# Kernel optimization log

Hardware: AMD Instinct MI355X
Metric: run time of the kernel (lower is better)

The kernel has to match this reference:

```python
import jax, jax.numpy as jnp
import numpy as np

N_NODES = 100000
N_EDGES = 1600000
IN_DIM = 128
HID = 128
OUT = 40


def setup_inputs() -> dict:
    key = jax.random.key(0)
    ks = jax.random.split(key, 8)
    x = jax.random.normal(ks[0], (N_NODES, IN_DIM), dtype=jnp.float32)
    edge_index = jax.random.randint(ks[1], (2, N_EDGES), 0, N_NODES, dtype=jnp.int64)
    def glorot(k, fan_in, fan_out):
        s = jnp.sqrt(6.0 / (fan_in + fan_out)).astype(jnp.float32)
        return jax.random.uniform(k, (fan_in, fan_out), jnp.float32, -s, s)
    return {
        "x": x,
        "edge_index": edge_index,
        "W1": glorot(ks[2], IN_DIM, HID), "b1": jnp.zeros((HID,), jnp.float32),
        "W2": glorot(ks[3], HID, HID),    "b2": jnp.zeros((HID,), jnp.float32),
        "W3": glorot(ks[4], HID, HID),    "b3": jnp.zeros((HID,), jnp.float32),
        "Wl": glorot(ks[5], HID, OUT),    "bl": jnp.zeros((OUT,), jnp.float32),
    }


def _gcn_norm(edge_index, num_nodes):
    # PyG GCNConv default: add self-loops, symmetric normalization.
    loops = jnp.arange(num_nodes, dtype=edge_index.dtype)
    src = jnp.concatenate([edge_index[0], loops])
    dst = jnp.concatenate([edge_index[1], loops])
    deg = jax.ops.segment_sum(jnp.ones_like(dst, dtype=jnp.float32), dst,
                              num_segments=num_nodes)
    dis = jnp.where(deg > 0, jax.lax.rsqrt(deg), 0.0)  # deg^{-1/2}
    norm = dis[src] * dis[dst]  # [E+N]
    return src, dst, norm


def _gcn_conv(x, W, b, src, dst, norm, num_nodes):
    h = x @ W                                   # [N, F_out]
    msg = h[src] * norm[:, None]                # gather + scale
    out = jax.ops.segment_sum(msg, dst, num_segments=num_nodes)
    return out + b


def reference(x, edge_index, W1, b1, W2, b2, W3, b3, Wl, bl):
    n = x.shape[0]
    src, dst, norm = _gcn_norm(edge_index, n)
    h = jax.nn.relu(_gcn_conv(x, W1, b1, src, dst, norm, n))
    h = jax.nn.relu(_gcn_conv(h, W2, b2, src, dst, norm, n))
    h = _gcn_conv(h, W3, b3, src, dst, norm, n)
    # dropout p=0.5 is identity in eval mode
    return h @ Wl + bl
```

## Files before the change

### kernel.cpp

```cpp
#include <hip/hip_runtime.h>

typedef __attribute__((ext_vector_type(8))) short sh8;
typedef __attribute__((ext_vector_type(4))) float f4;

__device__ __forceinline__ float bf2f(unsigned short u) {
    union { unsigned int u; float f; } c; c.u = ((unsigned int)u) << 16; return c.f;
}
__device__ __forceinline__ unsigned short f2bf(float f) {
    union { float f; unsigned int u; } c; c.f = f;
    unsigned int x = c.u;
    unsigned int r = (x + 0x7fffu + ((x >> 16) & 1u)) >> 16;
    return (unsigned short)r;
}
__device__ __forceinline__ void bfsplit(float x, short& hi, short& lo) {
    unsigned short h = f2bf(x);
    float r = x - bf2f(h);
    hi = (short)h;
    lo = (short)f2bf(r);
}

__global__ void k_zero_cnt(int* cnt, int N) {
    int i = blockIdx.x * 256 + threadIdx.x;
    if (i < N) cnt[i] = 0;
}

__global__ void k_count(const int* __restrict__ dst, int* __restrict__ cnt,
                        int* __restrict__ rank, int E, int N) {
    int E4 = E >> 2;
    for (int i = blockIdx.x * 256 + threadIdx.x; i < E4; i += gridDim.x * 256) {
        int4 d = ((const int4*)dst)[i];
        int4 r;
        r.x = ((unsigned)d.x < (unsigned)N) ? atomicAdd(&cnt[d.x], 1) : -1;
        r.y = ((unsigned)d.y < (unsigned)N) ? atomicAdd(&cnt[d.y], 1) : -1;
        r.z = ((unsigned)d.z < (unsigned)N) ? atomicAdd(&cnt[d.z], 1) : -1;
        r.w = ((unsigned)d.w < (unsigned)N) ? atomicAdd(&cnt[d.w], 1) : -1;
        ((int4*)rank)[i] = r;
    }
    if (blockIdx.x == 0) {
        for (int e = (E4 << 2) + threadIdx.x; e < E; e += 256) {
            int d = dst[e];
            rank[e] = ((unsigned)d < (unsigned)N) ? atomicAdd(&cnt[d], 1) : -1;
        }
    }
}

#define SCAN_B 256
__global__ void k_scan_a(const int* __restrict__ cnt, int* __restrict__ rowptr,
                         int* __restrict__ bsum, float* __restrict__ dis, int N) {
    __shared__ int sh[SCAN_B];
    int t = threadIdx.x, i = blockIdx.x * SCAN_B + t;
    int v = (i < N) ? cnt[i] : 0;
    if (i < N) dis[i] = rsqrtf((float)(v + 1));
    sh[t] = v; __syncthreads();
    for (int off = 1; off < SCAN_B; off <<= 1) {
        int x = (t >= off) ? sh[t - off] : 0;
        __syncthreads();
        sh[t] += x;
        __syncthreads();
    }
    int incl = sh[t];
    if (i < N) rowptr[i] = incl - v;
    if (t == SCAN_B - 1) bsum[blockIdx.x] = incl;
}

__global__ void k_scan_b(int* bsum, int NB) {
    __shared__ int sh[512];
    int t = threadIdx.x;
    int v = (t < NB) ? bsum[t] : 0;
    sh[t] = v; __syncthreads();
    for (int off = 1; off < 512; off <<= 1) {
        int x = (t >= off) ? sh[t - off] : 0;
        __syncthreads();
        sh[t] += x;
        __syncthreads();
    }
    if (t < NB) bsum[t] = sh[t] - v;
}

__global__ void k_scan_c(int* __restrict__ rowptr, const int* __restrict__ bsum, int N) {
    int i = blockIdx.x * 256 + threadIdx.x;
    if (i < N) rowptr[i] += bsum[blockIdx.x];
}

__global__ void k_fill(const int* __restrict__ src, const int* __restrict__ dst,
                       const int* __restrict__ rank, const int* __restrict__ rowptr,
                       int* __restrict__ csrc, int E, int N) {
    int E4 = E >> 2;
    for (int i = blockIdx.x * 256 + threadIdx.x; i < E4; i += gridDim.x * 256) {
        int4 d4 = ((const int4*)dst)[i];
        int4 s4 = ((const int4*)src)[i];
        int4 r4 = ((const int4*)rank)[i];
        #pragma unroll
        for (int q = 0; q < 4; ++q) {
            int d = (q == 0) ? d4.x : (q == 1) ? d4.y : (q == 2) ? d4.z : d4.w;
            int s = (q == 0) ? s4.x : (q == 1) ? s4.y : (q == 2) ? s4.z : s4.w;
            int r = (q == 0) ? r4.x : (q == 1) ? r4.y : (q == 2) ? r4.z : r4.w;
            if ((unsigned)d >= (unsigned)N || (unsigned)s >= (unsigned)N || r < 0) continue;
            csrc[rowptr[d] + r] = s;
        }
    }
    if (blockIdx.x == 0) {
        for (int e = (E4 << 2) + threadIdx.x; e < E; e += 256) {
            int d = dst[e];
            int s = src[e];
            int r = rank[e];
            if ((unsigned)d >= (unsigned)N || (unsigned)s >= (unsigned)N || r < 0) continue;
            csrc[rowptr[d] + r] = s;
        }
    }
}

__global__ __launch_bounds__(256)
void k_gemm128_a32(const float* __restrict__ X,
                   const float* __restrict__ W,
                   const float* __restrict__ dis,
                   unsigned short* __restrict__ H, int nPairs) {
    int wave = threadIdx.x >> 6;
    int lane = threadIdx.x & 63;
    int ln = lane & 15, quad = lane >> 4;
    int c0 = (wave & 1) * 64;
    int subTile = wave >> 1;

    sh8 bh[4][4], blo[4][4];
    #pragma unroll
    for (int nt = 0; nt < 4; ++nt) {
        int col = c0 + nt * 16 + ln;
        #pragma unroll
        for (int kt = 0; kt < 4; ++kt) {
            int k0 = kt * 32 + quad * 8;
            #pragma unroll
            for (int j = 0; j < 8; ++j) {
                short h, l;
                bfsplit(W[(k0 + j) * 128 + col], h, l);
                bh[nt][kt][j] = h; blo[nt][kt][j] = l;
            }
        }
    }

    for (int p = blockIdx.x; p < nPairs; p += gridDim.x) {
        int nodeBase = p * 32 + subTile * 16;
        const float* xrow = X + (nodeBase + ln) * 128 + quad * 8;
        sh8 ah[4], al[4];
        #pragma unroll
        for (int kt = 0; kt < 4; ++kt) {
            f4 v0 = *(const f4*)(xrow + kt * 32);
            f4 v1 = *(const f4*)(xrow + kt * 32 + 4);
            #pragma unroll
            for (int j = 0; j < 4; ++j) {
                short h, l;
                bfsplit(v0[j], h, l); ah[kt][j] = h; al[kt][j] = l;
                bfsplit(v1[j], h, l); ah[kt][j + 4] = h; al[kt][j + 4] = l;
            }
        }

        f4 acc[4] = { {0.f,0.f,0.f,0.f}, {0.f,0.f,0.f,0.f}, {0.f,0.f,0.f,0.f}, {0.f,0.f,0.f,0.f} };
        #pragma unroll
        for (int kt = 0; kt < 4; ++kt)
            #pragma unroll
            for (int nt = 0; nt < 4; ++nt) {
                acc[nt] = __builtin_amdgcn_mfma_f32_16x16x32_bf16(ah[kt], bh[nt][kt], acc[nt], 0, 0, 0);
                acc[nt] = __builtin_amdgcn_mfma_f32_16x16x32_bf16(ah[kt], blo[nt][kt], acc[nt], 0, 0, 0);
                acc[nt] = __builtin_amdgcn_mfma_f32_16x16x32_bf16(al[kt], bh[nt][kt], acc[nt], 0, 0, 0);
            }

        float ds[4];
        #pragma unroll
        for (int r = 0; r < 4; ++r) ds[r] = dis[nodeBase + quad * 4 + r];
        #pragma unroll
        for (int nt = 0; nt < 4; ++nt) {
            int col = c0 + nt * 16 + ln;
            #pragma unroll
            for (int r = 0; r < 4; ++r)
                H[(nodeBase + quad * 4 + r) * 128 + col] = f2bf(acc[nt][r] * ds[r]);
        }
    }
}

__global__ __launch_bounds__(256)
void k_gemm128_a16(const unsigned short* __restrict__ X,
                   const float* __restrict__ W,
                   const float* __restrict__ dis,
                   unsigned short* __restrict__ H, int nPairs) {
    int wave = threadIdx.x >> 6;
    int lane = threadIdx.x & 63;
    int ln = lane & 15, quad = lane >> 4;
    int c0 = (wave & 1) * 64;
    int subTile = wave >> 1;

    sh8 bh[4][4], blo[4][4];
    #pragma unroll
    for (int nt = 0; nt < 4; ++nt) {
        int col = c0 + nt * 16 + ln;
        #pragma unroll
        for (int kt = 0; kt < 4; ++kt) {
            int k0 = kt * 32 + quad * 8;
            #pragma unroll
            for (int j = 0; j < 8; ++j) {
                short h, l;
                bfsplit(W[(k0 + j) * 128 + col], h, l);
                bh[nt][kt][j] = h; blo[nt][kt][j] = l;
            }
        }
    }

    for (int p = blockIdx.x; p < nPairs; p += gridDim.x) {
        int nodeBase = p * 32 + subTile * 16;
        const unsigned short* xrow = X + (nodeBase + ln) * 128 + quad * 8;
        sh8 a[4];
        #pragma unroll
        for (int kt = 0; kt < 4; ++kt) a[kt] = *(const sh8*)(xrow + kt * 32);

        f4 acc[4] = { {0.f,0.f,0.f,0.f}, {0.f,0.f,0.f,0.f}, {0.f,0.f,0.f,0.f}, {0.f,0.f,0.f,0.f} };
        #pragma unroll
        for (int kt = 0; kt < 4; ++kt)
            #pragma unroll
            for (int nt = 0; nt < 4; ++nt) {
                acc[nt] = __builtin_amdgcn_mfma_f32_16x16x32_bf16(a[kt], bh[nt][kt], acc[nt], 0, 0, 0);
                acc[nt] = __builtin_amdgcn_mfma_f32_16x16x32_bf16(a[kt], blo[nt][kt], acc[nt], 0, 0, 0);
            }

        float ds[4];
        #pragma unroll
        for (int r = 0; r < 4; ++r) ds[r] = dis[nodeBase + quad * 4 + r];
        #pragma unroll
        for (int nt = 0; nt < 4; ++nt) {
            int col = c0 + nt * 16 + ln;
            #pragma unroll
            for (int r = 0; r < 4; ++r)
                H[(nodeBase + quad * 4 + r) * 128 + col] = f2bf(acc[nt][r] * ds[r]);
        }
    }
}

__global__ __launch_bounds__(256)
void k_agg(const unsigned short* __restrict__ H,
           unsigned short* __restrict__ O,
           const float* __restrict__ dis,
           const int* __restrict__ rowptr,
           const int* __restrict__ cnt,
           const int* __restrict__ csrc,
           const float* __restrict__ bias,
           int relu, int N) {
    int n = (blockIdx.x * 256 + threadIdx.x) >> 5;
    if (n >= N) return;
    int lane = threadIdx.x & 31;
    int sub  = lane & 15;
    int half = lane >> 4;

    float a0 = 0.f, a1 = 0.f, a2 = 0.f, a3 = 0.f;
    float a4 = 0.f, a5 = 0.f, a6 = 0.f, a7 = 0.f;

    auto addrow = [&](uint4 v) {
        a0 += bf2f((unsigned short)v.x);
        a1 += bf2f((unsigned short)(v.x >> 16));
        a2 += bf2f((unsigned short)v.y);
        a3 += bf2f((unsigned short)(v.y >> 16));
        a4 += bf2f((unsigned short)v.z);
        a5 += bf2f((unsigned short)(v.z >> 16));
        a6 += bf2f((unsigned short)v.w);
        a7 += bf2f((unsigned short)(v.w >> 16));
    };

    if (half == 0)
        addrow(*(const uint4*)(H + (size_t)n * 128 + sub * 8));

    int start = rowptr[n];
    int e = cnt[n];
    int i = 0;
    for (; i + 8 <= e; i += 8) {
        int s[4];
        #pragma unroll
        for (int q = 0; q < 4; ++q) s[q] = csrc[start + i + 2 * q + half];
        uint4 v[4];
        #pragma unroll
        for (int q = 0; q < 4; ++q) v[q] = *(const uint4*)(H + (size_t)s[q] * 128 + sub * 8);
        #pragma unroll
        for (int q = 0; q < 4; ++q) addrow(v[q]);
    }
    for (int j = i + half; j < e; j += 2) {
        int s = csrc[start + j];
        addrow(*(const uint4*)(H + (size_t)s * 128 + sub * 8));
    }

    a0 += __shfl_xor(a0, 16); a1 += __shfl_xor(a1, 16);
    a2 += __shfl_xor(a2, 16); a3 += __shfl_xor(a3, 16);
    a4 += __shfl_xor(a4, 16); a5 += __shfl_xor(a5, 16);
    a6 += __shfl_xor(a6, 16); a7 += __shfl_xor(a7, 16);

    if (half == 0) {
        float dn = dis[n];
        f4 b0 = *(const f4*)(bias + sub * 8);
        f4 b1 = *(const f4*)(bias + sub * 8 + 4);
        a0 = a0 * dn + b0[0]; a1 = a1 * dn + b0[1];
        a2 = a2 * dn + b0[2]; a3 = a3 * dn + b0[3];
        a4 = a4 * dn + b1[0]; a5 = a5 * dn + b1[1];
        a6 = a6 * dn + b1[2]; a7 = a7 * dn + b1[3];
        if (relu) {
            a0 = fmaxf(a0, 0.f); a1 = fmaxf(a1, 0.f);
            a2 = fmaxf(a2, 0.f); a3 = fmaxf(a3, 0.f);
            a4 = fmaxf(a4, 0.f); a5 = fmaxf(a5, 0.f);
            a6 = fmaxf(a6, 0.f); a7 = fmaxf(a7, 0.f);
        }
        uint4 ov;
        ov.x = (unsigned int)f2bf(a0) | ((unsigned int)f2bf(a1) << 16);
        ov.y = (unsigned int)f2bf(a2) | ((unsigned int)f2bf(a3) << 16);
        ov.z = (unsigned int)f2bf(a4) | ((unsigned int)f2bf(a5) << 16);
        ov.w = (unsigned int)f2bf(a6) | ((unsigned int)f2bf(a7) << 16);
        *(uint4*)(O + (size_t)n * 128 + sub * 8) = ov;
    }
}

__global__ __launch_bounds__(256)
void k_gemm_final(const unsigned short* __restrict__ X,
                  const float* __restrict__ W,
                  const float* __restrict__ bl,
                  float* __restrict__ OUT, int nTiles) {
    int wave = threadIdx.x >> 6;
    int lane = threadIdx.x & 63;
    int ln = lane & 15, quad = lane >> 4;
    int tile = blockIdx.x * 4 + wave;
    if (tile >= nTiles) return;

    sh8 bh[3][4], blo[3][4];
    #pragma unroll
    for (int nt = 0; nt < 3; ++nt) {
        int col = nt * 16 + ln;
        bool valid = (col < 40);
        #pragma unroll
        for (int kt = 0; kt < 4; ++kt) {
            int k0 = kt * 32 + quad * 8;
            #pragma unroll
            for (int j = 0; j < 8; ++j) {
                short h = 0, l = 0;
                if (valid) bfsplit(W[(k0 + j) * 40 + col], h, l);
                bh[nt][kt][j] = h; blo[nt][kt][j] = l;
            }
        }
    }

    int nodeBase = tile * 16;
    const unsigned short* xrow = X + (nodeBase + ln) * 128 + quad * 8;
    sh8 a[4];
    #pragma unroll
    for (int kt = 0; kt < 4; ++kt) a[kt] = *(const sh8*)(xrow + kt * 32);

    f4 acc[3] = { {0.f,0.f,0.f,0.f}, {0.f,0.f,0.f,0.f}, {0.f,0.f,0.f,0.f} };
    #pragma unroll
    for (int kt = 0; kt < 4; ++kt)
        #pragma unroll
        for (int nt = 0; nt < 3; ++nt) {
            acc[nt] = __builtin_amdgcn_mfma_f32_16x16x32_bf16(a[kt], bh[nt][kt], acc[nt], 0, 0, 0);
            acc[nt] = __builtin_amdgcn_mfma_f32_16x16x32_bf16(a[kt], blo[nt][kt], acc[nt], 0, 0, 0);
        }

    #pragma unroll
    for (int nt = 0; nt < 3; ++nt) {
        int col = nt * 16 + ln;
        if (col < 40) {
            float bv = bl[col];
            #pragma unroll
            for (int r = 0; r < 4; ++r)
                OUT[(nodeBase + quad * 4 + r) * 40 + col] = acc[nt][r] + bv;
        }
    }
}

extern "C" void kernel_launch(void* const* d_in, const int* in_sizes, int n_in,
                              void* d_out, int out_size, void* d_ws, size_t ws_size,
                              hipStream_t stream) {
    const float* x  = (const float*)d_in[0];
    const int*   ei = (const int*)d_in[1];
    const float* W1 = (const float*)d_in[2];
    const float* b1 = (const float*)d_in[3];
    const float* W2 = (const float*)d_in[4];
    const float* b2 = (const float*)d_in[5];
    const float* W3 = (const float*)d_in[6];
    const float* b3 = (const float*)d_in[7];
    const float* Wl = (const float*)d_in[8];
    const float* bl = (const float*)d_in[9];

    const int N = in_sizes[0] / 128;
    const int E = in_sizes[1] / 2;
    const int* srcIdx = ei;
    const int* dstIdx = ei + E;

    char* ws = (char*)d_ws;
    size_t off = 0;
    auto alloc = [&](size_t bytes) { void* p = ws + off; off += (bytes + 511) & ~(size_t)511; return p; };
    int*   cnt     = (int*)  alloc((size_t)N * 4);
    int*   rowptr  = (int*)  alloc((size_t)N * 4);
    float* dis     = (float*)alloc((size_t)N * 4);
    int*   bsum    = (int*)  alloc(512 * 4);
    int*   csrc    = (int*)  alloc((size_t)E * 4);
    unsigned short* h0 = (unsigned short*)alloc((size_t)N * 128 * 2);
    unsigned short* h1 = (unsigned short*)alloc((size_t)N * 128 * 2);
    int* rank = (int*)h0;

    const int gN = (N + 255) / 256;
    const int nPairs = N / 32;
    const int nTiles = N / 16;
    const int gAgg = (N * 32 + 255) / 256;

    k_zero_cnt<<<gN, 256, 0, stream>>>(cnt, N);
    k_count<<<1568, 256, 0, stream>>>(dstIdx, cnt, rank, E, N);
    k_scan_a<<<gN, 256, 0, stream>>>(cnt, rowptr, bsum, dis, N);
    k_scan_b<<<1, 512, 0, stream>>>(bsum, gN);
    k_scan_c<<<gN, 256, 0, stream>>>(rowptr, bsum, N);
    k_fill<<<1568, 256, 0, stream>>>(srcIdx, dstIdx, rank, rowptr, csrc, E, N);

    k_gemm128_a32<<<768, 256, 0, stream>>>(x, W1, dis, h0, nPairs);
    k_agg<<<gAgg, 256, 0, stream>>>(h0, h1, dis, rowptr, cnt, csrc, b1, 1, N);
    k_gemm128_a16<<<768, 256, 0, stream>>>(h1, W2, dis, h0, nPairs);
    k_agg<<<gAgg, 256, 0, stream>>>(h0, h1, dis, rowptr, cnt, csrc, b2, 1, N);
    k_gemm128_a16<<<768, 256, 0, stream>>>(h1, W3, dis, h0, nPairs);
    k_agg<<<gAgg, 256, 0, stream>>>(h0, h1, dis, rowptr, cnt, csrc, b3, 0, N);
    k_gemm_final<<<(nTiles + 3) / 4, 256, 0, stream>>>(h1, Wl, bl, (float*)d_out, nTiles);
}
```

Before: 492.1 us.

## Privatize CSR degree counters into eight replicas to cut atomic contention

Degree counting now uses eight replicated counter arrays, each indexed by block id modulo 8, so concurrent atomics on the same destination node are spread across copies. The scan sums the replicas to get the degree, writes per-replica offsets, and the fill kernel uses the replica offset that matches the block that produced each rank. This aims to reduce atomic serialization during CSR construction. The cost is eight times more counter memory and scan traffic, and correctness relies on the fill kernel's block-to-replica mapping matching the count kernel's exactly.

```diff
diff --git a/kernel.cpp b/kernel.cpp
--- a/kernel.cpp
+++ b/kernel.cpp
@@ -19,38 +19,48 @@
     lo = (short)f2bf(r);
 }
 
-__global__ void k_zero_cnt(int* cnt, int N) {
+#define CSR_GRID 1568
+
+__global__ void k_zero_cnt(int* cnt, int M) {
     int i = blockIdx.x * 256 + threadIdx.x;
-    if (i < N) cnt[i] = 0;
-}
-
-__global__ void k_count(const int* __restrict__ dst, int* __restrict__ cnt,
+    if (i < M) cnt[i] = 0;
+}
+
+__global__ void k_count(const int* __restrict__ dst, int* __restrict__ cnt8,
                         int* __restrict__ rank, int E, int N) {
+    int base = (blockIdx.x & 7) * N;
     int E4 = E >> 2;
     for (int i = blockIdx.x * 256 + threadIdx.x; i < E4; i += gridDim.x * 256) {
         int4 d = ((const int4*)dst)[i];
         int4 r;
-        r.x = ((unsigned)d.x < (unsigned)N) ? atomicAdd(&cnt[d.x], 1) : -1;
-        r.y = ((unsigned)d.y < (unsigned)N) ? atomicAdd(&cnt[d.y], 1) : -1;
-        r.z = ((unsigned)d.z < (unsigned)N) ? atomicAdd(&cnt[d.z], 1) : -1;
-        r.w = ((unsigned)d.w < (unsigned)N) ? atomicAdd(&cnt[d.w], 1) : -1;
+        r.x = ((unsigned)d.x < (unsigned)N) ? atomicAdd(&cnt8[base + d.x], 1) : -1;
+        r.y = ((unsigned)d.y < (unsigned)N) ? atomicAdd(&cnt8[base + d.y], 1) : -1;
+        r.z = ((unsigned)d.z < (unsigned)N) ? atomicAdd(&cnt8[base + d.z], 1) : -1;
+        r.w = ((unsigned)d.w < (unsigned)N) ? atomicAdd(&cnt8[base + d.w], 1) : -1;
         ((int4*)rank)[i] = r;
     }
     if (blockIdx.x == 0) {
         for (int e = (E4 << 2) + threadIdx.x; e < E; e += 256) {
             int d = dst[e];
-            rank[e] = ((unsigned)d < (unsigned)N) ? atomicAdd(&cnt[d], 1) : -1;
+            rank[e] = ((unsigned)d < (unsigned)N) ? atomicAdd(&cnt8[d], 1) : -1;
         }
     }
 }
 
 #define SCAN_B 256
-__global__ void k_scan_a(const int* __restrict__ cnt, int* __restrict__ rowptr,
+__global__ void k_scan_a(const int* __restrict__ cnt8, int* __restrict__ rowptr,
+                         int* __restrict__ off8, int* __restrict__ deg,
                          int* __restrict__ bsum, float* __restrict__ dis, int N) {
     __shared__ int sh[SCAN_B];
     int t = threadIdx.x, i = blockIdx.x * SCAN_B + t;
-    int v = (i < N) ? cnt[i] : 0;
-    if (i < N) dis[i] = rsqrtf((float)(v + 1));
+    int c[8];
+    int v = 0;
+    if (i < N) {
+        #pragma unroll
+        for (int g = 0; g < 8; ++g) { c[g] = cnt8[g * N + i]; v += c[g]; }
+        dis[i] = rsqrtf((float)(v + 1));
+        deg[i] = v;
+    }
     sh[t] = v; __syncthreads();
     for (int off = 1; off < SCAN_B; off <<= 1) {
         int x = (t >= off) ? sh[t - off] : 0;
@@ -59,7 +69,13 @@
         __syncthreads();
     }
     int incl = sh[t];
-    if (i < N) rowptr[i] = incl - v;
+    if (i < N) {
+        int b = incl - v;
+        rowptr[i] = b;
+        int o = b;
+        #pragma unroll
+        for (int g = 0; g < 8; ++g) { off8[g * N + i] = o; o += c[g]; }
+    }
     if (t == SCAN_B - 1) bsum[blockIdx.x] = incl;
 }
 
@@ -77,16 +93,24 @@
     if (t < NB) bsum[t] = sh[t] - v;
 }
 
-__global__ void k_scan_c(int* __restrict__ rowptr, const int* __restrict__ bsum, int N) {
+__global__ void k_scan_c(int* __restrict__ rowptr, int* __restrict__ off8,
+                         const int* __restrict__ bsum, int N) {
     int i = blockIdx.x * 256 + threadIdx.x;
-    if (i < N) rowptr[i] += bsum[blockIdx.x];
+    if (i < N) {
+        int b = bsum[blockIdx.x];
+        rowptr[i] += b;
+        #pragma unroll
+        for (int g = 0; g < 8; ++g) off8[g * N + i] += b;
+    }
 }
 
 __global__ void k_fill(const int* __restrict__ src, const int* __restrict__ dst,
-                       const int* __restrict__ rank, const int* __restrict__ rowptr,
+                       const int* __restrict__ rank, const int* __restrict__ off8,
                        int* __restrict__ csrc, int E, int N) {
     int E4 = E >> 2;
     for (int i = blockIdx.x * 256 + threadIdx.x; i < E4; i += gridDim.x * 256) {
+        int g = ((i >> 8) % gridDim.x) & 7;
+        const int* off = off8 + g * N;
         int4 d4 = ((const int4*)dst)[i];
         int4 s4 = ((const int4*)src)[i];
         int4 r4 = ((const int4*)rank)[i];
@@ -96,7 +120,7 @@
             int s = (q == 0) ? s4.x : (q == 1) ? s4.y : (q == 2) ? s4.z : s4.w;
             int r = (q == 0) ? r4.x : (q == 1) ? r4.y : (q == 2) ? r4.z : r4.w;
             if ((unsigned)d >= (unsigned)N || (unsigned)s >= (unsigned)N || r < 0) continue;
-            csrc[rowptr[d] + r] = s;
+            csrc[off[d] + r] = s;
         }
     }
     if (blockIdx.x == 0) {
@@ -105,7 +129,7 @@
             int s = src[e];
             int r = rank[e];
             if ((unsigned)d >= (unsigned)N || (unsigned)s >= (unsigned)N || r < 0) continue;
-            csrc[rowptr[d] + r] = s;
+            csrc[off8[d] + r] = s;
         }
     }
 }
@@ -237,7 +261,7 @@
            unsigned short* __restrict__ O,
            const float* __restrict__ dis,
            const int* __restrict__ rowptr,
-           const int* __restrict__ cnt,
+           const int* __restrict__ deg,
            const int* __restrict__ csrc,
            const float* __restrict__ bias,
            int relu, int N) {
@@ -265,7 +289,7 @@
         addrow(*(const uint4*)(H + (size_t)n * 128 + sub * 8));
 
     int start = rowptr[n];
-    int e = cnt[n];
+    int e = deg[n];
     int i = 0;
     for (; i + 8 <= e; i += 8) {
         int s[4];
@@ -387,32 +411,35 @@
     char* ws = (char*)d_ws;
     size_t off = 0;
     auto alloc = [&](size_t bytes) { void* p = ws + off; off += (bytes + 511) & ~(size_t)511; return p; };
-    int*   cnt     = (int*)  alloc((size_t)N * 4);
     int*   rowptr  = (int*)  alloc((size_t)N * 4);
+    int*   deg     = (int*)  alloc((size_t)N * 4);
     float* dis     = (float*)alloc((size_t)N * 4);
     int*   bsum    = (int*)  alloc(512 * 4);
     int*   csrc    = (int*)  alloc((size_t)E * 4);
     unsigned short* h0 = (unsigned short*)alloc((size_t)N * 128 * 2);
     unsigned short* h1 = (unsigned short*)alloc((size_t)N * 128 * 2);
     int* rank = (int*)h0;
+    int* cnt8 = (int*)((char*)h0 + (8u << 20));
+    int* off8 = (int*)h1;
 
     const int gN = (N + 255) / 256;
     const int nPairs = N / 32;
     const int nTiles = N / 16;
     const int gAgg = (N * 32 + 255) / 256;
-
-    k_zero_cnt<<<gN, 256, 0, stream>>>(cnt, N);
-    k_count<<<1568, 256, 0, stream>>>(dstIdx, cnt, rank, E, N);
-    k_scan_a<<<gN, 256, 0, stream>>>(cnt, rowptr, bsum, dis, N);
+    const int gZ8 = (N * 8 + 255) / 256;
+
+    k_zero_cnt<<<gZ8, 256, 0, stream>>>(cnt8, N * 8);
+    k_count<<<CSR_GRID, 256, 0, stream>>>(dstIdx, cnt8, rank, E, N);
+    k_scan_a<<<gN, 256, 0, stream>>>(cnt8, rowptr, off8, deg, bsum, dis, N);
     k_scan_b<<<1, 512, 0, stream>>>(bsum, gN);
-    k_scan_c<<<gN, 256, 0, stream>>>(rowptr, bsum, N);
-    k_fill<<<1568, 256, 0, stream>>>(srcIdx, dstIdx, rank, rowptr, csrc, E, N);
+    k_scan_c<<<gN, 256, 0, stream>>>(rowptr, off8, bsum, N);
+    k_fill<<<CSR_GRID, 256, 0, stream>>>(srcIdx, dstIdx, rank, off8, csrc, E, N);
 
     k_gemm128_a32<<<768, 256, 0, stream>>>(x, W1, dis, h0, nPairs);
-    k_agg<<<gAgg, 256, 0, stream>>>(h0, h1, dis, rowptr, cnt, csrc, b1, 1, N);
+    k_agg<<<gAgg, 256, 0, stream>>>(h0, h1, dis, rowptr, deg, csrc, b1, 1, N);
     k_gemm128_a16<<<768, 256, 0, stream>>>(h1, W2, dis, h0, nPairs);
-    k_agg<<<gAgg, 256, 0, stream>>>(h0, h1, dis, rowptr, cnt, csrc, b2, 1, N);
+    k_agg<<<gAgg, 256, 0, stream>>>(h0, h1, dis, rowptr, deg, csrc, b2, 1, N);
     k_gemm128_a16<<<768, 256, 0, stream>>>(h1, W3, dis, h0, nPairs);
-    k_agg<<<gAgg, 256, 0, stream>>>(h0, h1, dis, rowptr, cnt, csrc, b3, 0, N);
+    k_agg<<<gAgg, 256, 0, stream>>>(h0, h1, dis, rowptr, deg, csrc, b3, 0, N);
     k_gemm_final<<<(nTiles + 3) / 4, 256, 0, stream>>>(h1, Wl, bl, (float*)d_out, nTiles);
 }
```

Result: no change. 492.9 us (+0.2%).
